# Kernel optimization log

Measured on AMD Instinct MI355X. Metric: run time of the kernel, lower is better.

The kernel has to match this reference:

```python
import jax, jax.numpy as jnp
import numpy as np

B, S, D, H = 2, 2048, 1024, 16
DH = D // H
ROPE_BASE = 10000.0


def apply_rope(x):
    # x: [B, H, S, DH]; rotate-half RoPE, base 10000
    half = DH // 2
    inv_freq = 1.0 / (ROPE_BASE ** (jnp.arange(half, dtype=jnp.float32) / half))
    ang = jnp.arange(S, dtype=jnp.float32)[:, None] * inv_freq[None, :]  # [S, half]
    cos = jnp.cos(ang)[None, None]  # [1,1,S,half]
    sin = jnp.sin(ang)[None, None]
    x1, x2 = x[..., :half], x[..., half:]
    return jnp.concatenate([x1 * cos - x2 * sin, x1 * sin + x2 * cos], axis=-1)


def setup_inputs() -> dict:
    key = jax.random.key(0)
    ks = jax.random.split(key, 9)
    w = lambda k: jax.random.normal(k, (D, D), dtype=jnp.float32) * 0.02
    return {
        "x": jax.random.normal(ks[0], (B, S, D), dtype=jnp.float32),
        "Wq": w(ks[1]), "bq": jnp.zeros((D,), jnp.float32),
        "Wk": w(ks[2]), "bk": jnp.zeros((D,), jnp.float32),
        "Wv": w(ks[3]), "bv": jnp.zeros((D,), jnp.float32),
        "Wo": w(ks[4]), "bo": jnp.zeros((D,), jnp.float32),
    }


def reference(x, Wq, bq, Wk, bk, Wv, bv, Wo, bo):
    # projections (W stored as [in, out])
    q = x @ Wq + bq
    k = x @ Wk + bk
    v = x @ Wv + bv
    # [B, S, D] -> [B, H, S, DH]
    to_heads = lambda t: t.reshape(B, S, H, DH).transpose(0, 2, 1, 3)
    q, k, v = to_heads(q), to_heads(k), to_heads(v)
    q = apply_rope(q)
    k = apply_rope(k)
    scores = jnp.einsum("bhqd,bhkd->bhqk", q, k) / jnp.sqrt(jnp.float32(DH))
    causal = jnp.tril(jnp.ones((S, S), dtype=bool))  # [S, S]
    scores = jnp.where(causal[None, None], scores, -jnp.inf)
    probs = jax.nn.softmax(scores, axis=-1)
    ctx = jnp.einsum("bhqk,bhkd->bhqd", probs, v)
    ctx = ctx.transpose(0, 2, 1, 3).reshape(B, S, D)  # concat heads
    return ctx @ Wo + bo
```

## Files before the change

### kernel.cpp

```cpp
#include <hip/hip_runtime.h>
#include <hip/hip_bf16.h>

#define B_  2
#define S_  2048
#define D_  1024
#define H_  16
#define DH_ 64

typedef __attribute__((ext_vector_type(8))) short bf16x8;
typedef __attribute__((ext_vector_type(4))) float f32x4;

__device__ __forceinline__ short f2bf(float f) {
  unsigned int u; __builtin_memcpy(&u, &f, 4);
  u = (u + 0x7FFFu + ((u >> 16) & 1u)) >> 16;
  return (short)u;
}
__device__ __forceinline__ unsigned cvtpk(float a, float b) {
  unsigned r;
  asm("v_cvt_pk_bf16_f32 %0, %1, %2" : "=v"(r) : "v"(a), "v"(b));
  return r;
}

#define GLOAD_LDS16(gp, lp) \
  __builtin_amdgcn_global_load_lds((const __attribute__((address_space(1))) void*)(gp), \
                                   (__attribute__((address_space(3))) void*)(lp), 16, 0, 0)

#define MFMA16(a, b, c) __builtin_amdgcn_mfma_f32_16x16x32_bf16(a, b, c, 0, 0, 0)

union U8 { unsigned u[4]; bf16x8 v; };

__global__ __launch_bounds__(256) void k_cvt(const float* __restrict__ in,
                                             short* __restrict__ out, int n4) {
  int i = blockIdx.x * 256 + threadIdx.x;
  if (i >= n4) return;
  float4 v = ((const float4*)in)[i];
  short4 o; o.x = f2bf(v.x); o.y = f2bf(v.y); o.z = f2bf(v.z); o.w = f2bf(v.w);
  *(short4*)(out + (size_t)i * 4) = o;
}

__global__ __launch_bounds__(256) void k_transpose4(const float* __restrict__ W0,
                                                    const float* __restrict__ W1,
                                                    const float* __restrict__ W2,
                                                    const float* __restrict__ W3,
                                                    short* __restrict__ WtBase) {
  __shared__ float tile[32][33];
  const float* W = (blockIdx.z == 0) ? W0 : (blockIdx.z == 1) ? W1 :
                   (blockIdx.z == 2) ? W2 : W3;
  short* Wt = WtBase + (size_t)blockIdx.z * D_ * D_;
  int tx = threadIdx.x, ty = threadIdx.y;
  int bx = blockIdx.x * 32, by = blockIdx.y * 32;
  #pragma unroll
  for (int i = 0; i < 32; i += 8)
    tile[ty + i][tx] = W[(size_t)(by + ty + i) * D_ + bx + tx];
  __syncthreads();
  #pragma unroll
  for (int i = 0; i < 32; i += 8)
    Wt[(size_t)(bx + ty + i) * D_ + by + tx] = f2bf(tile[tx][ty + i]);
}

__global__ __launch_bounds__(256) void k_rope_table(float* __restrict__ cosT,
                                                    float* __restrict__ sinT) {
  int i = blockIdx.x * 256 + threadIdx.x;
  int s = i >> 5, d = i & 31;
  float invf = exp2f(-(float)d * (13.287712379549449f / 32.0f));
  float ang = (float)s * invf;
  cosT[i] = cosf(ang);
  sinT[i] = sinf(ang);
}

__global__ __launch_bounds__(256) void k_gemm_qkv(const short* __restrict__ A,
                                                  const short* __restrict__ Bt,
                                                  const float* __restrict__ bq,
                                                  const float* __restrict__ bk,
                                                  const float* __restrict__ bv,
                                                  const float* __restrict__ cosT,
                                                  const float* __restrict__ sinT,
                                                  short* __restrict__ qb,
                                                  short* __restrict__ kb,
                                                  short* __restrict__ vb) {
  const int K = 1024;
  __shared__ __align__(16) short lA[128 * 32];
  __shared__ __align__(16) short lB[128 * 32];
  const int tid = threadIdx.x;
  const int wid = tid >> 6, lane = tid & 63;
  const int brow = blockIdx.y * 128, bcol = blockIdx.x * 128;
  const int wr = wid >> 1, wc = wid & 1;
  const int g = lane >> 4, c15 = lane & 15;
  const int sr = lane >> 2, scol = (lane & 3) * 8;
  f32x4 acc[4][4] = {};

  for (int kt = 0; kt < K; kt += 32) {
    __syncthreads();
    #pragma unroll
    for (int ch = 0; ch < 2; ++ch) {
      const short* ga = A + (size_t)(brow + ch * 64 + wid * 16 + sr) * K + kt + scol;
      const short* gb = Bt + (size_t)(bcol + ch * 64 + wid * 16 + sr) * K + kt + scol;
      GLOAD_LDS16(ga, &lA[(ch * 64 + wid * 16) * 32]);
      GLOAD_LDS16(gb, &lB[(ch * 64 + wid * 16) * 32]);
    }
    __syncthreads();
    bf16x8 af[4], bfr[4];
    #pragma unroll
    for (int mi = 0; mi < 4; ++mi)
      af[mi] = *(const bf16x8*)&lA[(wr * 64 + mi * 16 + c15) * 32 + g * 8];
    #pragma unroll
    for (int ni = 0; ni < 4; ++ni)
      bfr[ni] = *(const bf16x8*)&lB[(wc * 64 + ni * 16 + c15) * 32 + g * 8];
    #pragma unroll
    for (int mi = 0; mi < 4; ++mi)
      #pragma unroll
      for (int ni = 0; ni < 4; ++ni)
        acc[mi][ni] = MFMA16(af[mi], bfr[ni], acc[mi][ni]);
  }

  const int seg = bcol >> 10;
  const float* bp = (seg == 0) ? bq : (seg == 1) ? bk : bv;
  short* dst = (seg == 0) ? qb : (seg == 1) ? kb : vb;
  const float alpha = (seg == 0) ? 0.18033688f : 1.0f;
  const bool rope = (seg < 2);
  #pragma unroll
  for (int mi = 0; mi < 4; ++mi) {
    #pragma unroll
    for (int ni = 0; ni < 2; ++ni) {
      int col  = bcol + wc * 64 + ni * 16 + c15;
      int lcol = col & 1023;
      int d    = col & 63;
      float b1 = bp[lcol], b2 = bp[lcol + 32];
      #pragma unroll
      for (int r = 0; r < 4; ++r) {
        int row = brow + wr * 64 + mi * 16 + g * 4 + r;
        float x1 = (acc[mi][ni][r]     + b1) * alpha;
        float x2 = (acc[mi][ni + 2][r] + b2) * alpha;
        float o1 = x1, o2 = x2;
        if (rope) {
          int s = row & (S_ - 1);
          float co = cosT[s * 32 + d], si = sinT[s * 32 + d];
          o1 = x1 * co - x2 * si;
          o2 = x1 * si + x2 * co;
        }
        dst[(size_t)row * 1024 + lcol]      = f2bf(o1);
        dst[(size_t)row * 1024 + lcol + 32] = f2bf(o2);
      }
    }
  }
}

__global__ __launch_bounds__(256) void k_gemm(const short* __restrict__ A,
                                              const short* __restrict__ Bt,
                                              const float* __restrict__ bias,
                                              float* __restrict__ out,
                                              int M, int N, int K) {
  __shared__ __align__(16) short lA[128 * 32];
  __shared__ __align__(16) short lB[128 * 32];
  const int tid = threadIdx.x;
  const int wid = tid >> 6, lane = tid & 63;
  const int brow = blockIdx.y * 128, bcol = blockIdx.x * 128;
  const int wr = wid >> 1, wc = wid & 1;
  const int g = lane >> 4, c15 = lane & 15;
  const int sr = lane >> 2, scol = (lane & 3) * 8;
  f32x4 acc[4][4] = {};

  for (int kt = 0; kt < K; kt += 32) {
    __syncthreads();
    #pragma unroll
    for (int ch = 0; ch < 2; ++ch) {
      const short* ga = A + (size_t)(brow + ch * 64 + wid * 16 + sr) * K + kt + scol;
      const short* gb = Bt + (size_t)(bcol + ch * 64 + wid * 16 + sr) * K + kt + scol;
      GLOAD_LDS16(ga, &lA[(ch * 64 + wid * 16) * 32]);
      GLOAD_LDS16(gb, &lB[(ch * 64 + wid * 16) * 32]);
    }
    __syncthreads();
    bf16x8 af[4], bfr[4];
    #pragma unroll
    for (int mi = 0; mi < 4; ++mi)
      af[mi] = *(const bf16x8*)&lA[(wr * 64 + mi * 16 + c15) * 32 + g * 8];
    #pragma unroll
    for (int ni = 0; ni < 4; ++ni)
      bfr[ni] = *(const bf16x8*)&lB[(wc * 64 + ni * 16 + c15) * 32 + g * 8];
    #pragma unroll
    for (int mi = 0; mi < 4; ++mi)
      #pragma unroll
      for (int ni = 0; ni < 4; ++ni)
        acc[mi][ni] = MFMA16(af[mi], bfr[ni], acc[mi][ni]);
  }

  #pragma unroll
  for (int mi = 0; mi < 4; ++mi) {
    #pragma unroll
    for (int ni = 0; ni < 4; ++ni) {
      int col = bcol + wc * 64 + ni * 16 + c15;
      float bv = bias[col];
      #pragma unroll
      for (int r = 0; r < 4; ++r) {
        int row = brow + wr * 64 + mi * 16 + g * 4 + r;
        out[(size_t)row * N + col] = acc[mi][ni][r] + bv;
      }
    }
  }
}

__global__ __launch_bounds__(256) void k_flash(const short* __restrict__ Qb,
                                               const short* __restrict__ Kb,
                                               const short* __restrict__ Vb,
                                               short* __restrict__ Ctx,
                                               float* __restrict__ pO,
                                               float* __restrict__ pML) {
  __shared__ __align__(16) short Vt[2][64][72];
  __shared__ __align__(16) short Kl[2][4096];
  const int bid = blockIdx.x;
  const int sched = bid >> 5, bh = bid & 31;
  int qt, t0, t1, sid = 0; bool split;
  if (sched < 19) { qt = 18 - sched; t0 = 0; t1 = qt; split = false; }
  else {
    int j = sched - 19; qt = 31 - (j >> 1);
    int h1 = (qt + 2) >> 1;
    if ((j & 1) == 0) { t0 = h1; t1 = qt; }
    else              { t0 = 0;  t1 = h1 - 1; }
    split = true; sid = bh * 26 + j;
  }
  const int b   = bh >> 4, h = bh & 15;
  const int tid = threadIdx.x, w = tid >> 6, lane = tid & 63;
  const int g   = lane >> 4, c15 = lane & 15;
  const int qg0 = qt * 64 + w * 16;
  const int qabs = qg0 + c15;

  const short* qp = Qb + ((size_t)(b * S_ + qabs)) * D_ + h * DH_ + g * 8;
  bf16x8 qf0 = *(const bf16x8*)qp;
  bf16x8 qf1 = *(const bf16x8*)(qp + 32);

  const int vkv = lane;
  const int vd0 = w * 16;
  const int vcol = vkv ^ (w << 3);
  const short* vrow = Vb + (size_t)b * S_ * D_ + h * DH_ + vd0;

  const short* kbase = Kb + (size_t)b * S_ * D_ + h * DH_;
  const int kidx0 = w * 128 + lane;
  const int kkv0 = kidx0 >> 3, kdb0 = (kidx0 & 7) ^ (kkv0 & 7);
  const int kidx1 = kidx0 + 64;
  const int kkv1 = kidx1 >> 3, kdb1 = (kidx1 & 7) ^ (kkv1 & 7);

  f32x4 o[4] = {};
  float m = -1e30f, l = 0.0f;

  {
    const short* kb0 = kbase + (size_t)(t0 * 64) * D_;
    GLOAD_LDS16(kb0 + (size_t)kkv0 * D_ + kdb0 * 8, &Kl[t0 & 1][(w * 128) * 8]);
    GLOAD_LDS16(kb0 + (size_t)kkv1 * D_ + kdb1 * 8, &Kl[t0 & 1][(w * 128 + 64) * 8]);
    const short* vp = vrow + (size_t)(t0 * 64 + vkv) * D_;
    bf16x8 a = *(const bf16x8*)vp;
    bf16x8 c = *(const bf16x8*)(vp + 8);
    #pragma unroll
    for (int j = 0; j < 8; ++j) Vt[t0 & 1][vd0 + j][vcol] = a[j];
    #pragma unroll
    for (int j = 0; j < 8; ++j) Vt[t0 & 1][vd0 + 8 + j][vcol] = c[j];
  }
  __syncthreads();

  for (int t = t0; t <= t1; ++t) {
    const int kv0 = t * 64;
    bf16x8 nv0, nv1;
    if (t + 1 <= t1) {
      const short* kb2 = kbase + (size_t)(kv0 + 64) * D_;
      GLOAD_LDS16(kb2 + (size_t)kkv0 * D_ + kdb0 * 8, &Kl[(t + 1) & 1][(w * 128) * 8]);
      GLOAD_LDS16(kb2 + (size_t)kkv1 * D_ + kdb1 * 8, &Kl[(t + 1) & 1][(w * 128 + 64) * 8]);
      const short* vp = vrow + (size_t)(kv0 + 64 + vkv) * D_;
      nv0 = *(const bf16x8*)vp;
      nv1 = *(const bf16x8*)(vp + 8);
    }
    const short* ks = &Kl[t & 1][0];
    f32x4 s[4] = {};
    __builtin_amdgcn_s_setprio(1);
    #pragma unroll
    for (int n = 0; n < 4; ++n) {
      int krow = (n * 16 + c15) * 64;
      bf16x8 k0 = *(const bf16x8*)&ks[krow + ((g ^ (c15 & 7)) * 8)];
      bf16x8 k1 = *(const bf16x8*)&ks[krow + (((g + 4) ^ (c15 & 7)) * 8)];
      s[n] = MFMA16(k0, qf0, s[n]);
      s[n] = MFMA16(k1, qf1, s[n]);
    }
    __builtin_amdgcn_s_setprio(0);
    if (kv0 + 63 > qg0) {
      #pragma unroll
      for (int n = 0; n < 4; ++n)
        #pragma unroll
        for (int r = 0; r < 4; ++r)
          if (kv0 + n * 16 + g * 4 + r > qabs) s[n][r] = -1e30f;
    }
    float pm = -1e30f;
    #pragma unroll
    for (int n = 0; n < 4; ++n)
      #pragma unroll
      for (int r = 0; r < 4; ++r) pm = fmaxf(pm, s[n][r]);
    pm = fmaxf(pm, __shfl_xor(pm, 16));
    pm = fmaxf(pm, __shfl_xor(pm, 32));
    if (!__all(pm <= m + 8.0f)) {
      float nm = fmaxf(m, pm);
      float corr = exp2f(m - nm);
      m = nm; l *= corr;
      float cf[4];
      #pragma unroll
      for (int r = 0; r < 4; ++r) cf[r] = __shfl(corr, g * 4 + r);
      #pragma unroll
      for (int dblk = 0; dblk < 4; ++dblk)
        #pragma unroll
        for (int r = 0; r < 4; ++r) o[dblk][r] *= cf[r];
    }
    float rs = 0.0f;
    #pragma unroll
    for (int n = 0; n < 4; ++n)
      #pragma unroll
      for (int r = 0; r < 4; ++r) {
        float p = exp2f(s[n][r] - m);
        s[n][r] = p; rs += p;
      }
    rs += __shfl_xor(rs, 16);
    rs += __shfl_xor(rs, 32);
    l += rs;
    unsigned pk[4][2];
    #pragma unroll
    for (int n = 0; n < 4; ++n) {
      pk[n][0] = cvtpk(s[n][0], s[n][1]);
      pk[n][1] = cvtpk(s[n][2], s[n][3]);
    }
    U8 pa[2];
    #pragma unroll
    for (int kh = 0; kh < 2; ++kh) {
      #pragma unroll
      for (int widx = 0; widx < 4; ++widx) {
        int src = (2 * (g & 1) + (widx >> 1)) * 16 + c15;
        unsigned lo = __shfl(pk[2 * kh][widx & 1], src);
        unsigned hi = __shfl(pk[2 * kh + 1][widx & 1], src);
        pa[kh].u[widx] = (g & 2) ? hi : lo;
      }
    }
    __builtin_amdgcn_s_setprio(1);
    #pragma unroll
    for (int kh = 0; kh < 2; ++kh)
      #pragma unroll
      for (int dblk = 0; dblk < 4; ++dblk) {
        bf16x8 vbf = *(const bf16x8*)&Vt[t & 1][dblk * 16 + c15][kh * 32 + ((g ^ dblk) * 8)];
        o[dblk] = MFMA16(pa[kh].v, vbf, o[dblk]);
      }
    __builtin_amdgcn_s_setprio(0);
    if (t + 1 <= t1) {
      #pragma unroll
      for (int j = 0; j < 8; ++j) Vt[(t + 1) & 1][vd0 + j][vcol] = nv0[j];
      #pragma unroll
      for (int j = 0; j < 8; ++j) Vt[(t + 1) & 1][vd0 + 8 + j][vcol] = nv1[j];
    }
    __syncthreads();
  }

  if (!split) {
    float linv = 1.0f / l;
    float lf[4];
    #pragma unroll
    for (int r = 0; r < 4; ++r) lf[r] = __shfl(linv, g * 4 + r);
    #pragma unroll
    for (int dblk = 0; dblk < 4; ++dblk)
      #pragma unroll
      for (int r = 0; r < 4; ++r) {
        int q = qg0 + g * 4 + r;
        Ctx[((size_t)(b * S_ + q)) * D_ + h * DH_ + dblk * 16 + c15] = f2bf(o[dblk][r] * lf[r]);
      }
  } else {
    float* po = pO + ((size_t)sid * 64 + w * 16) * 64;
    #pragma unroll
    for (int dblk = 0; dblk < 4; ++dblk)
      #pragma unroll
      for (int r = 0; r < 4; ++r)
        po[(g * 4 + r) * 64 + dblk * 16 + c15] = o[dblk][r];
    if (lane < 16) {
      pML[(size_t)sid * 128 + w * 16 + lane]      = m;
      pML[(size_t)sid * 128 + 64 + w * 16 + lane] = l;
    }
  }
}

__global__ __launch_bounds__(256) void k_combine(const float* __restrict__ pO,
                                                 const float* __restrict__ pML,
                                                 short* __restrict__ Ctx) {
  const int p = blockIdx.x;
  const int qt = 19 + (p >> 5), bh = p & 31;
  const int b = bh >> 4, h = bh & 15;
  const int jb = (31 - qt) * 2;
  const int sidB = bh * 26 + jb;
  const int sidA = bh * 26 + jb + 1;
  const int q = threadIdx.x >> 2;
  const int d0 = (threadIdx.x & 3) * 16;
  float mA = pML[(size_t)sidA * 128 + q], lA = pML[(size_t)sidA * 128 + 64 + q];
  float mB = pML[(size_t)sidB * 128 + q], lB = pML[(size_t)sidB * 128 + 64 + q];
  float M = fmaxf(mA, mB);
  float wA = exp2f(mA - M), wB = exp2f(mB - M);
  float inv = 1.0f / (lA * wA + lB * wB);
  const float* oA = pO + ((size_t)sidA * 64 + q) * 64 + d0;
  const float* oB = pO + ((size_t)sidB * 64 + q) * 64 + d0;
  short* cp = Ctx + ((size_t)(b * S_ + qt * 64 + q)) * D_ + h * DH_ + d0;
  #pragma unroll
  for (int i = 0; i < 16; i += 4) {
    float4 a = *(const float4*)(oA + i);
    float4 c = *(const float4*)(oB + i);
    cp[i + 0] = f2bf((a.x * wA + c.x * wB) * inv);
    cp[i + 1] = f2bf((a.y * wA + c.y * wB) * inv);
    cp[i + 2] = f2bf((a.z * wA + c.z * wB) * inv);
    cp[i + 3] = f2bf((a.w * wA + c.w * wB) * inv);
  }
}

extern "C" void kernel_launch(void* const* d_in, const int* in_sizes, int n_in,
                              void* d_out, int out_size, void* d_ws, size_t ws_size,
                              hipStream_t stream) {
  (void)in_sizes; (void)n_in; (void)out_size; (void)ws_size;
  const float* x  = (const float*)d_in[0];
  const float* Wq = (const float*)d_in[1];
  const float* bq = (const float*)d_in[2];
  const float* Wk = (const float*)d_in[3];
  const float* bk = (const float*)d_in[4];
  const float* Wv = (const float*)d_in[5];
  const float* bv = (const float*)d_in[6];
  const float* Wo = (const float*)d_in[7];
  const float* bo = (const float*)d_in[8];
  float* out = (float*)d_out;
  char* ws = (char*)d_ws;

  const size_t MS = (size_t)B_ * S_;
  short* xb  = (short*)(ws);
  short* wqT = (short*)(ws + (size_t)8 * 1024 * 1024);
  short* wkT = wqT + (size_t)D_ * D_;
  short* wvT = wkT + (size_t)D_ * D_;
  short* woT = wvT + (size_t)D_ * D_;
  short* qb  = (short*)(ws + (size_t)16 * 1024 * 1024);
  short* kb  = qb + MS * D_;
  short* vb  = kb + MS * D_;
  short* ctx = vb + MS * D_;
  float* cosT = (float*)(ws + (size_t)48 * 1024 * 1024);
  float* sinT = cosT + (size_t)S_ * 32;
  float* pO  = (float*)(ws);
  float* pML = (float*)(ws + (size_t)48 * 1024 * 1024 + 512 * 1024);

  k_cvt<<<dim3((unsigned)(MS * D_ / 4 / 256)), 256, 0, stream>>>(x, xb, (int)(MS * D_ / 4));
  k_transpose4<<<dim3(32, 32, 4), dim3(32, 8), 0, stream>>>(Wq, Wk, Wv, Wo, wqT);
  k_rope_table<<<dim3(S_ * 32 / 256), 256, 0, stream>>>(cosT, sinT);
  k_gemm_qkv<<<dim3(24, 32), 256, 0, stream>>>(xb, wqT, bq, bk, bv, cosT, sinT, qb, kb, vb);
  k_flash<<<dim3(45 * 32), 256, 0, stream>>>(qb, kb, vb, ctx, pO, pML);
  k_combine<<<dim3(13 * 32), 256, 0, stream>>>(pO, pML, ctx);
  k_gemm<<<dim3(8, 32), 256, 0, stream>>>(ctx, woT, bo, out, 4096, 1024, 1024);
}
```

Before: 138.5 us.

## Double query rows per flash block to reuse K/V tiles, re-plan split schedule

```diff
diff --git a/kernel.cpp b/kernel.cpp
--- a/kernel.cpp
+++ b/kernel.cpp
@@ -199,34 +199,92 @@
   }
 }
 
-__global__ __launch_bounds__(256) void k_flash(const short* __restrict__ Qb,
-                                               const short* __restrict__ Kb,
-                                               const short* __restrict__ Vb,
-                                               short* __restrict__ Ctx,
-                                               float* __restrict__ pO,
-                                               float* __restrict__ pML) {
+__device__ __forceinline__ void softmax_g(f32x4 (&s)[4], float& m, float& l,
+                                          f32x4 (&o)[4], int g) {
+  float pm = -1e30f;
+  #pragma unroll
+  for (int n = 0; n < 4; ++n)
+    #pragma unroll
+    for (int r = 0; r < 4; ++r) pm = fmaxf(pm, s[n][r]);
+  pm = fmaxf(pm, __shfl_xor(pm, 16));
+  pm = fmaxf(pm, __shfl_xor(pm, 32));
+  if (!__all(pm <= m + 8.0f)) {
+    float nm = fmaxf(m, pm);
+    float corr = exp2f(m - nm);
+    m = nm; l *= corr;
+    float cf[4];
+    #pragma unroll
+    for (int r = 0; r < 4; ++r) cf[r] = __shfl(corr, g * 4 + r);
+    #pragma unroll
+    for (int dblk = 0; dblk < 4; ++dblk)
+      #pragma unroll
+      for (int r = 0; r < 4; ++r) o[dblk][r] *= cf[r];
+  }
+  float rs = 0.0f;
+  #pragma unroll
+  for (int n = 0; n < 4; ++n)
+    #pragma unroll
+    for (int r = 0; r < 4; ++r) {
+      float p = exp2f(s[n][r] - m);
+      s[n][r] = p; rs += p;
+    }
+  rs += __shfl_xor(rs, 16);
+  rs += __shfl_xor(rs, 32);
+  l += rs;
+}
+
+__device__ __forceinline__ void build_pa(const f32x4 (&s)[4], U8 (&pa)[2],
+                                         int g, int c15) {
+  unsigned pk[4][2];
+  #pragma unroll
+  for (int n = 0; n < 4; ++n) {
+    pk[n][0] = cvtpk(s[n][0], s[n][1]);
+    pk[n][1] = cvtpk(s[n][2], s[n][3]);
+  }
+  #pragma unroll
+  for (int kh = 0; kh < 2; ++kh) {
+    #pragma unroll
+    for (int widx = 0; widx < 4; ++widx) {
+      int src = (2 * (g & 1) + (widx >> 1)) * 16 + c15;
+      unsigned lo = __shfl(pk[2 * kh][widx & 1], src);
+      unsigned hi = __shfl(pk[2 * kh + 1][widx & 1], src);
+      pa[kh].u[widx] = (g & 2) ? hi : lo;
+    }
+  }
+}
+
+__global__ __launch_bounds__(256, 4) void k_flash(const short* __restrict__ Qb,
+                                                  const short* __restrict__ Kb,
+                                                  const short* __restrict__ Vb,
+                                                  short* __restrict__ Ctx,
+                                                  float* __restrict__ pO,
+                                                  float* __restrict__ pML) {
   __shared__ __align__(16) short Vt[2][64][72];
   __shared__ __align__(16) short Kl[2][4096];
   const int bid = blockIdx.x;
   const int sched = bid >> 5, bh = bid & 31;
-  int qt, t0, t1, sid = 0; bool split;
-  if (sched < 19) { qt = 18 - sched; t0 = 0; t1 = qt; split = false; }
-  else {
-    int j = sched - 19; qt = 31 - (j >> 1);
-    int h1 = (qt + 2) >> 1;
-    if ((j & 1) == 0) { t0 = h1; t1 = qt; }
-    else              { t0 = 0;  t1 = h1 - 1; }
-    split = true; sid = bh * 26 + j;
-  }
+  const unsigned char QTs[23] = {8,15,15,7,14,14,6,13,13,12,12,5,11,11,10,10,4,9,9,3,2,1,0};
+  const unsigned char MDs[23] = {0,1, 2, 0,1, 2, 0,1, 2, 1, 2, 0,1, 2, 1, 2, 0,1,2,0,0,0,0};
+  const int qt = QTs[sched], md = MDs[sched];
+  int t0, t1;
+  if (md == 0)      { t0 = 0;      t1 = 2 * qt + 1; }
+  else if (md == 1) { t0 = 0;      t1 = qt; }
+  else              { t0 = qt + 1; t1 = 2 * qt + 1; }
+  const bool split = (md != 0);
+  const int sid = bh * 14 + (qt - 9) * 2 + (md == 2 ? 1 : 0);
   const int b   = bh >> 4, h = bh & 15;
   const int tid = threadIdx.x, w = tid >> 6, lane = tid & 63;
   const int g   = lane >> 4, c15 = lane & 15;
-  const int qg0 = qt * 64 + w * 16;
-  const int qabs = qg0 + c15;
-
-  const short* qp = Qb + ((size_t)(b * S_ + qabs)) * D_ + h * DH_ + g * 8;
-  bf16x8 qf0 = *(const bf16x8*)qp;
-  bf16x8 qf1 = *(const bf16x8*)(qp + 32);
+  const int qg0a = qt * 128 + w * 32;
+  const int qabsA = qg0a + c15;
+  const int qabsB = qg0a + 16 + c15;
+
+  const short* qpA = Qb + ((size_t)(b * S_ + qabsA)) * D_ + h * DH_ + g * 8;
+  const short* qpB = Qb + ((size_t)(b * S_ + qabsB)) * D_ + h * DH_ + g * 8;
+  bf16x8 qfa0 = *(const bf16x8*)qpA;
+  bf16x8 qfa1 = *(const bf16x8*)(qpA + 32);
+  bf16x8 qfb0 = *(const bf16x8*)qpB;
+  bf16x8 qfb1 = *(const bf16x8*)(qpB + 32);
 
   const int vkv = lane;
   const int vd0 = w * 16;
@@ -239,8 +297,8 @@
   const int kidx1 = kidx0 + 64;
   const int kkv1 = kidx1 >> 3, kdb1 = (kidx1 & 7) ^ (kkv1 & 7);
 
-  f32x4 o[4] = {};
-  float m = -1e30f, l = 0.0f;
+  f32x4 oa[4] = {}, ob[4] = {};
+  float ma = -1e30f, la = 0.0f, mb = -1e30f, lb = 0.0f;
 
   {
     const short* kb0 = kbase + (size_t)(t0 * 64) * D_;
@@ -267,112 +325,90 @@
       nv0 = *(const bf16x8*)vp;
       nv1 = *(const bf16x8*)(vp + 8);
     }
-    const short* ks = &Kl[t & 1][0];
-    f32x4 s[4] = {};
-    __builtin_amdgcn_s_setprio(1);
-    #pragma unroll
-    for (int n = 0; n < 4; ++n) {
-      int krow = (n * 16 + c15) * 64;
-      bf16x8 k0 = *(const bf16x8*)&ks[krow + ((g ^ (c15 & 7)) * 8)];
-      bf16x8 k1 = *(const bf16x8*)&ks[krow + (((g + 4) ^ (c15 & 7)) * 8)];
-      s[n] = MFMA16(k0, qf0, s[n]);
-      s[n] = MFMA16(k1, qf1, s[n]);
-    }
-    __builtin_amdgcn_s_setprio(0);
-    if (kv0 + 63 > qg0) {
-      #pragma unroll
-      for (int n = 0; n < 4; ++n)
+    const bool liveB = (kv0 <= qg0a + 31);
+    if (liveB) {
+      const bool liveA = (kv0 <= qg0a + 15);
+      const short* ks = &Kl[t & 1][0];
+      f32x4 sa[4] = {}, sb[4] = {};
+      __builtin_amdgcn_s_setprio(1);
+      #pragma unroll
+      for (int n = 0; n < 4; ++n) {
+        int krow = (n * 16 + c15) * 64;
+        bf16x8 k0 = *(const bf16x8*)&ks[krow + ((g ^ (c15 & 7)) * 8)];
+        bf16x8 k1 = *(const bf16x8*)&ks[krow + (((g + 4) ^ (c15 & 7)) * 8)];
+        sa[n] = MFMA16(k0, qfa0, sa[n]);
+        sa[n] = MFMA16(k1, qfa1, sa[n]);
+        sb[n] = MFMA16(k0, qfb0, sb[n]);
+        sb[n] = MFMA16(k1, qfb1, sb[n]);
+      }
+      __builtin_amdgcn_s_setprio(0);
+      if (kv0 + 63 > qg0a) {
         #pragma unroll
-        for (int r = 0; r < 4; ++r)
-          if (kv0 + n * 16 + g * 4 + r > qabs) s[n][r] = -1e30f;
-    }
-    float pm = -1e30f;
-    #pragma unroll
-    for (int n = 0; n < 4; ++n)
-      #pragma unroll
-      for (int r = 0; r < 4; ++r) pm = fmaxf(pm, s[n][r]);
-    pm = fmaxf(pm, __shfl_xor(pm, 16));
-    pm = fmaxf(pm, __shfl_xor(pm, 32));
-    if (!__all(pm <= m + 8.0f)) {
-      float nm = fmaxf(m, pm);
-      float corr = exp2f(m - nm);
-      m = nm; l *= corr;
-      float cf[4];
-      #pragma unroll
-      for (int r = 0; r < 4; ++r) cf[r] = __shfl(corr, g * 4 + r);
-      #pragma unroll
-      for (int dblk = 0; dblk < 4; ++dblk)
+        for (int n = 0; n < 4; ++n)
+          #pragma unroll
+          for (int r = 0; r < 4; ++r)
+            if (kv0 + n * 16 + g * 4 + r > qabsA) sa[n][r] = -1e30f;
+      }
+      if (kv0 + 63 > qg0a + 16) {
         #pragma unroll
-        for (int r = 0; r < 4; ++r) o[dblk][r] *= cf[r];
-    }
-    float rs = 0.0f;
-    #pragma unroll
-    for (int n = 0; n < 4; ++n)
+        for (int n = 0; n < 4; ++n)
+          #pragma unroll
+          for (int r = 0; r < 4; ++r)
+            if (kv0 + n * 16 + g * 4 + r > qabsB) sb[n][r] = -1e30f;
+      }
+      U8 paa[2], pab[2];
+      if (liveA) { softmax_g(sa, ma, la, oa, g); build_pa(sa, paa, g, c15); }
+      softmax_g(sb, mb, lb, ob, g); build_pa(sb, pab, g, c15);
+      __builtin_amdgcn_s_setprio(1);
+      #pragma unroll
+      for (int kh = 0; kh < 2; ++kh)
+        #pragma unroll
+        for (int dblk = 0; dblk < 4; ++dblk) {
+          bf16x8 vbf = *(const bf16x8*)&Vt[t & 1][dblk * 16 + c15][kh * 32 + ((g ^ dblk) * 8)];
+          if (liveA) oa[dblk] = MFMA16(paa[kh].v, vbf, oa[dblk]);
+          ob[dblk] = MFMA16(pab[kh].v, vbf, ob[dblk]);
+        }
+      __builtin_amdgcn_s_setprio(0);
+    }
+    if (t + 1 <= t1) {
+      #pragma unroll
+      for (int j = 0; j < 8; ++j) Vt[(t + 1) & 1][vd0 + j][vcol] = nv0[j];
+      #pragma unroll
+      for (int j = 0; j < 8; ++j) Vt[(t + 1) & 1][vd0 + 8 + j][vcol] = nv1[j];
+    }
+    __syncthreads();
+  }
+
+  if (!split) {
+    float liA = 1.0f / la, liB = 1.0f / lb;
+    float lfA[4], lfB[4];
+    #pragma unroll
+    for (int r = 0; r < 4; ++r) {
+      lfA[r] = __shfl(liA, g * 4 + r);
+      lfB[r] = __shfl(liB, g * 4 + r);
+    }
+    #pragma unroll
+    for (int dblk = 0; dblk < 4; ++dblk)
       #pragma unroll
       for (int r = 0; r < 4; ++r) {
-        float p = exp2f(s[n][r] - m);
-        s[n][r] = p; rs += p;
-      }
-    rs += __shfl_xor(rs, 16);
-    rs += __shfl_xor(rs, 32);
-    l += rs;
-    unsigned pk[4][2];
-    #pragma unroll
-    for (int n = 0; n < 4; ++n) {
-      pk[n][0] = cvtpk(s[n][0], s[n][1]);
-      pk[n][1] = cvtpk(s[n][2], s[n][3]);
-    }
-    U8 pa[2];
-    #pragma unroll
-    for (int kh = 0; kh < 2; ++kh) {
-      #pragma unroll
-      for (int widx = 0; widx < 4; ++widx) {
-        int src = (2 * (g & 1) + (widx >> 1)) * 16 + c15;
-        unsigned lo = __shfl(pk[2 * kh][widx & 1], src);
-        unsigned hi = __shfl(pk[2 * kh + 1][widx & 1], src);
-        pa[kh].u[widx] = (g & 2) ? hi : lo;
-      }
-    }
-    __builtin_amdgcn_s_setprio(1);
-    #pragma unroll
-    for (int kh = 0; kh < 2; ++kh)
-      #pragma unroll
-      for (int dblk = 0; dblk < 4; ++dblk) {
-        bf16x8 vbf = *(const bf16x8*)&Vt[t & 1][dblk * 16 + c15][kh * 32 + ((g ^ dblk) * 8)];
-        o[dblk] = MFMA16(pa[kh].v, vbf, o[dblk]);
-      }
-    __builtin_amdgcn_s_setprio(0);
-    if (t + 1 <= t1) {
-      #pragma unroll
-      for (int j = 0; j < 8; ++j) Vt[(t + 1) & 1][vd0 + j][vcol] = nv0[j];
-      #pragma unroll
-      for (int j = 0; j < 8; ++j) Vt[(t + 1) & 1][vd0 + 8 + j][vcol] = nv1[j];
-    }
-    __syncthreads();
-  }
-
-  if (!split) {
-    float linv = 1.0f / l;
-    float lf[4];
-    #pragma unroll
-    for (int r = 0; r < 4; ++r) lf[r] = __shfl(linv, g * 4 + r);
+        int qa = qg0a + g * 4 + r;
+        Ctx[((size_t)(b * S_ + qa)) * D_ + h * DH_ + dblk * 16 + c15] = f2bf(oa[dblk][r] * lfA[r]);
+        Ctx[((size_t)(b * S_ + qa + 16)) * D_ + h * DH_ + dblk * 16 + c15] = f2bf(ob[dblk][r] * lfB[r]);
+      }
+  } else {
+    float* po = pO + ((size_t)sid * 128 + w * 32) * 64;
     #pragma unroll
     for (int dblk = 0; dblk < 4; ++dblk)
       #pragma unroll
       for (int r = 0; r < 4; ++r) {
-        int q = qg0 + g * 4 + r;
-        Ctx[((size_t)(b * S_ + q)) * D_ + h * DH_ + dblk * 16 + c15] = f2bf(o[dblk][r] * lf[r]);
-      }
-  } else {
-    float* po = pO + ((size_t)sid * 64 + w * 16) * 64;
-    #pragma unroll
-    for (int dblk = 0; dblk < 4; ++dblk)
-      #pragma unroll
-      for (int r = 0; r < 4; ++r)
-        po[(g * 4 + r) * 64 + dblk * 16 + c15] = o[dblk][r];
+        po[(g * 4 + r) * 64 + dblk * 16 + c15]        = oa[dblk][r];
+        po[(16 + g * 4 + r) * 64 + dblk * 16 + c15]   = ob[dblk][r];
+      }
     if (lane < 16) {
-      pML[(size_t)sid * 128 + w * 16 + lane]      = m;
-      pML[(size_t)sid * 128 + 64 + w * 16 + lane] = l;
+      pML[(size_t)sid * 256 + w * 32 + lane]            = ma;
+      pML[(size_t)sid * 256 + 128 + w * 32 + lane]      = la;
+      pML[(size_t)sid * 256 + w * 32 + 16 + lane]       = mb;
+      pML[(size_t)sid * 256 + 128 + w * 32 + 16 + lane] = lb;
     }
   }
 }
@@ -381,23 +417,22 @@
                                                  const float* __restrict__ pML,
                                                  short* __restrict__ Ctx) {
   const int p = blockIdx.x;
-  const int qt = 19 + (p >> 5), bh = p & 31;
+  const int qt = 9 + (p >> 5), bh = p & 31;
   const int b = bh >> 4, h = bh & 15;
-  const int jb = (31 - qt) * 2;
-  const int sidB = bh * 26 + jb;
-  const int sidA = bh * 26 + jb + 1;
-  const int q = threadIdx.x >> 2;
-  const int d0 = (threadIdx.x & 3) * 16;
-  float mA = pML[(size_t)sidA * 128 + q], lA = pML[(size_t)sidA * 128 + 64 + q];
-  float mB = pML[(size_t)sidB * 128 + q], lB = pML[(size_t)sidB * 128 + 64 + q];
+  const int sidA = bh * 14 + (qt - 9) * 2;
+  const int sidB = sidA + 1;
+  const int row = threadIdx.x >> 1;
+  const int d0 = (threadIdx.x & 1) * 32;
+  float mA = pML[(size_t)sidA * 256 + row], lA = pML[(size_t)sidA * 256 + 128 + row];
+  float mB = pML[(size_t)sidB * 256 + row], lB = pML[(size_t)sidB * 256 + 128 + row];
   float M = fmaxf(mA, mB);
   float wA = exp2f(mA - M), wB = exp2f(mB - M);
   float inv = 1.0f / (lA * wA + lB * wB);
-  const float* oA = pO + ((size_t)sidA * 64 + q) * 64 + d0;
-  const float* oB = pO + ((size_t)sidB * 64 + q) * 64 + d0;
-  short* cp = Ctx + ((size_t)(b * S_ + qt * 64 + q)) * D_ + h * DH_ + d0;
-  #pragma unroll
-  for (int i = 0; i < 16; i += 4) {
+  const float* oA = pO + ((size_t)sidA * 128 + row) * 64 + d0;
+  const float* oB = pO + ((size_t)sidB * 128 + row) * 64 + d0;
+  short* cp = Ctx + ((size_t)(b * S_ + qt * 128 + row)) * D_ + h * DH_ + d0;
+  #pragma unroll
+  for (int i = 0; i < 32; i += 4) {
     float4 a = *(const float4*)(oA + i);
     float4 c = *(const float4*)(oB + i);
     cp[i + 0] = f2bf((a.x * wA + c.x * wB) * inv);
@@ -442,7 +477,7 @@
   k_transpose4<<<dim3(32, 32, 4), dim3(32, 8), 0, stream>>>(Wq, Wk, Wv, Wo, wqT);
   k_rope_table<<<dim3(S_ * 32 / 256), 256, 0, stream>>>(cosT, sinT);
   k_gemm_qkv<<<dim3(24, 32), 256, 0, stream>>>(xb, wqT, bq, bk, bv, cosT, sinT, qb, kb, vb);
-  k_flash<<<dim3(45 * 32), 256, 0, stream>>>(qb, kb, vb, ctx, pO, pML);
-  k_combine<<<dim3(13 * 32), 256, 0, stream>>>(pO, pML, ctx);
+  k_flash<<<dim3(23 * 32), 256, 0, stream>>>(qb, kb, vb, ctx, pO, pML);
+  k_combine<<<dim3(7 * 32), 256, 0, stream>>>(pO, pML, ctx);
   k_gemm<<<dim3(8, 32), 256, 0, stream>>>(ctx, woT, bo, out, 4096, 1024, 1024);
 }
```

Result: slower. 162.7 us (+17.5%).

## Use 128-row query tiles with 8-wave flash blocks and rebalanced split schedule

Applied to the files above, without the earlier changes.

```diff
diff --git a/kernel.cpp b/kernel.cpp
--- a/kernel.cpp
+++ b/kernel.cpp
@@ -199,7 +199,61 @@
   }
 }
 
-__global__ __launch_bounds__(256) void k_flash(const short* __restrict__ Qb,
+__device__ __forceinline__ void softmax_g(f32x4 (&s)[4], float& m, float& l,
+                                          f32x4 (&o)[4], int g) {
+  float pm = -1e30f;
+  #pragma unroll
+  for (int n = 0; n < 4; ++n)
+    #pragma unroll
+    for (int r = 0; r < 4; ++r) pm = fmaxf(pm, s[n][r]);
+  pm = fmaxf(pm, __shfl_xor(pm, 16));
+  pm = fmaxf(pm, __shfl_xor(pm, 32));
+  if (!__all(pm <= m + 8.0f)) {
+    float nm = fmaxf(m, pm);
+    float corr = exp2f(m - nm);
+    m = nm; l *= corr;
+    float cf[4];
+    #pragma unroll
+    for (int r = 0; r < 4; ++r) cf[r] = __shfl(corr, g * 4 + r);
+    #pragma unroll
+    for (int dblk = 0; dblk < 4; ++dblk)
+      #pragma unroll
+      for (int r = 0; r < 4; ++r) o[dblk][r] *= cf[r];
+  }
+  float rs = 0.0f;
+  #pragma unroll
+  for (int n = 0; n < 4; ++n)
+    #pragma unroll
+    for (int r = 0; r < 4; ++r) {
+      float p = exp2f(s[n][r] - m);
+      s[n][r] = p; rs += p;
+    }
+  rs += __shfl_xor(rs, 16);
+  rs += __shfl_xor(rs, 32);
+  l += rs;
+}
+
+__device__ __forceinline__ void build_pa(const f32x4 (&s)[4], U8 (&pa)[2],
+                                         int g, int c15) {
+  unsigned pk[4][2];
+  #pragma unroll
+  for (int n = 0; n < 4; ++n) {
+    pk[n][0] = cvtpk(s[n][0], s[n][1]);
+    pk[n][1] = cvtpk(s[n][2], s[n][3]);
+  }
+  #pragma unroll
+  for (int kh = 0; kh < 2; ++kh) {
+    #pragma unroll
+    for (int widx = 0; widx < 4; ++widx) {
+      int src = (2 * (g & 1) + (widx >> 1)) * 16 + c15;
+      unsigned lo = __shfl(pk[2 * kh][widx & 1], src);
+      unsigned hi = __shfl(pk[2 * kh + 1][widx & 1], src);
+      pa[kh].u[widx] = (g & 2) ? hi : lo;
+    }
+  }
+}
+
+__global__ __launch_bounds__(512) void k_flash(const short* __restrict__ Qb,
                                                const short* __restrict__ Kb,
                                                const short* __restrict__ Vb,
                                                short* __restrict__ Ctx,
@@ -209,19 +263,19 @@
   __shared__ __align__(16) short Kl[2][4096];
   const int bid = blockIdx.x;
   const int sched = bid >> 5, bh = bid & 31;
-  int qt, t0, t1, sid = 0; bool split;
-  if (sched < 19) { qt = 18 - sched; t0 = 0; t1 = qt; split = false; }
-  else {
-    int j = sched - 19; qt = 31 - (j >> 1);
-    int h1 = (qt + 2) >> 1;
-    if ((j & 1) == 0) { t0 = h1; t1 = qt; }
-    else              { t0 = 0;  t1 = h1 - 1; }
-    split = true; sid = bh * 26 + j;
-  }
+  const unsigned char QTs[22] = {9,8,15,15,7,14,14,6,13,13,12,12,5,11,11,10,10,4,3,2,1,0};
+  const unsigned char MDs[22] = {0,0,1, 2, 0,1, 2, 0,1, 2, 1, 2, 0,1, 2, 1, 2, 0,0,0,0,0};
+  const int qt = QTs[sched], md = MDs[sched];
+  int t0, t1;
+  if (md == 0)      { t0 = 0;      t1 = 2 * qt + 1; }
+  else if (md == 1) { t0 = 0;      t1 = qt; }
+  else              { t0 = qt + 1; t1 = 2 * qt + 1; }
+  const bool split = (md != 0);
+  const int sid = bh * 12 + (qt - 10) * 2 + (md == 2 ? 1 : 0);
   const int b   = bh >> 4, h = bh & 15;
   const int tid = threadIdx.x, w = tid >> 6, lane = tid & 63;
   const int g   = lane >> 4, c15 = lane & 15;
-  const int qg0 = qt * 64 + w * 16;
+  const int qg0 = qt * 128 + w * 16;
   const int qabs = qg0 + c15;
 
   const short* qp = Qb + ((size_t)(b * S_ + qabs)) * D_ + h * DH_ + g * 8;
@@ -229,124 +283,71 @@
   bf16x8 qf1 = *(const bf16x8*)(qp + 32);
 
   const int vkv = lane;
-  const int vd0 = w * 16;
-  const int vcol = vkv ^ (w << 3);
+  const int vd0 = w * 8;
+  const int vcol = vkv ^ ((w >> 1) << 3);
   const short* vrow = Vb + (size_t)b * S_ * D_ + h * DH_ + vd0;
 
   const short* kbase = Kb + (size_t)b * S_ * D_ + h * DH_;
-  const int kidx0 = w * 128 + lane;
-  const int kkv0 = kidx0 >> 3, kdb0 = (kidx0 & 7) ^ (kkv0 & 7);
-  const int kidx1 = kidx0 + 64;
-  const int kkv1 = kidx1 >> 3, kdb1 = (kidx1 & 7) ^ (kkv1 & 7);
+  const int kidx = w * 64 + lane;
+  const int kkv = kidx >> 3, kdb = (kidx & 7) ^ (kkv & 7);
 
   f32x4 o[4] = {};
   float m = -1e30f, l = 0.0f;
 
   {
     const short* kb0 = kbase + (size_t)(t0 * 64) * D_;
-    GLOAD_LDS16(kb0 + (size_t)kkv0 * D_ + kdb0 * 8, &Kl[t0 & 1][(w * 128) * 8]);
-    GLOAD_LDS16(kb0 + (size_t)kkv1 * D_ + kdb1 * 8, &Kl[t0 & 1][(w * 128 + 64) * 8]);
+    GLOAD_LDS16(kb0 + (size_t)kkv * D_ + kdb * 8, &Kl[t0 & 1][kidx * 8]);
     const short* vp = vrow + (size_t)(t0 * 64 + vkv) * D_;
     bf16x8 a = *(const bf16x8*)vp;
-    bf16x8 c = *(const bf16x8*)(vp + 8);
     #pragma unroll
     for (int j = 0; j < 8; ++j) Vt[t0 & 1][vd0 + j][vcol] = a[j];
-    #pragma unroll
-    for (int j = 0; j < 8; ++j) Vt[t0 & 1][vd0 + 8 + j][vcol] = c[j];
   }
   __syncthreads();
 
   for (int t = t0; t <= t1; ++t) {
     const int kv0 = t * 64;
-    bf16x8 nv0, nv1;
+    bf16x8 nv;
     if (t + 1 <= t1) {
       const short* kb2 = kbase + (size_t)(kv0 + 64) * D_;
-      GLOAD_LDS16(kb2 + (size_t)kkv0 * D_ + kdb0 * 8, &Kl[(t + 1) & 1][(w * 128) * 8]);
-      GLOAD_LDS16(kb2 + (size_t)kkv1 * D_ + kdb1 * 8, &Kl[(t + 1) & 1][(w * 128 + 64) * 8]);
-      const short* vp = vrow + (size_t)(kv0 + 64 + vkv) * D_;
-      nv0 = *(const bf16x8*)vp;
-      nv1 = *(const bf16x8*)(vp + 8);
-    }
-    const short* ks = &Kl[t & 1][0];
-    f32x4 s[4] = {};
-    __builtin_amdgcn_s_setprio(1);
-    #pragma unroll
-    for (int n = 0; n < 4; ++n) {
-      int krow = (n * 16 + c15) * 64;
-      bf16x8 k0 = *(const bf16x8*)&ks[krow + ((g ^ (c15 & 7)) * 8)];
-      bf16x8 k1 = *(const bf16x8*)&ks[krow + (((g + 4) ^ (c15 & 7)) * 8)];
-      s[n] = MFMA16(k0, qf0, s[n]);
-      s[n] = MFMA16(k1, qf1, s[n]);
-    }
-    __builtin_amdgcn_s_setprio(0);
-    if (kv0 + 63 > qg0) {
-      #pragma unroll
-      for (int n = 0; n < 4; ++n)
+      GLOAD_LDS16(kb2 + (size_t)kkv * D_ + kdb * 8, &Kl[(t + 1) & 1][kidx * 8]);
+      nv = *(const bf16x8*)(vrow + (size_t)(kv0 + 64 + vkv) * D_);
+    }
+    if (kv0 <= qg0 + 15) {
+      const short* ks = &Kl[t & 1][0];
+      f32x4 s[4] = {};
+      __builtin_amdgcn_s_setprio(1);
+      #pragma unroll
+      for (int n = 0; n < 4; ++n) {
+        int krow = (n * 16 + c15) * 64;
+        bf16x8 k0 = *(const bf16x8*)&ks[krow + ((g ^ (c15 & 7)) * 8)];
+        bf16x8 k1 = *(const bf16x8*)&ks[krow + (((g + 4) ^ (c15 & 7)) * 8)];
+        s[n] = MFMA16(k0, qf0, s[n]);
+        s[n] = MFMA16(k1, qf1, s[n]);
+      }
+      __builtin_amdgcn_s_setprio(0);
+      if (kv0 + 63 > qg0) {
         #pragma unroll
-        for (int r = 0; r < 4; ++r)
-          if (kv0 + n * 16 + g * 4 + r > qabs) s[n][r] = -1e30f;
-    }
-    float pm = -1e30f;
-    #pragma unroll
-    for (int n = 0; n < 4; ++n)
-      #pragma unroll
-      for (int r = 0; r < 4; ++r) pm = fmaxf(pm, s[n][r]);
-    pm = fmaxf(pm, __shfl_xor(pm, 16));
-    pm = fmaxf(pm, __shfl_xor(pm, 32));
-    if (!__all(pm <= m + 8.0f)) {
-      float nm = fmaxf(m, pm);
-      float corr = exp2f(m - nm);
-      m = nm; l *= corr;
-      float cf[4];
-      #pragma unroll
-      for (int r = 0; r < 4; ++r) cf[r] = __shfl(corr, g * 4 + r);
-      #pragma unroll
-      for (int dblk = 0; dblk < 4; ++dblk)
+        for (int n = 0; n < 4; ++n)
+          #pragma unroll
+          for (int r = 0; r < 4; ++r)
+            if (kv0 + n * 16 + g * 4 + r > qabs) s[n][r] = -1e30f;
+      }
+      softmax_g(s, m, l, o, g);
+      U8 pa[2];
+      build_pa(s, pa, g, c15);
+      __builtin_amdgcn_s_setprio(1);
+      #pragma unroll
+      for (int kh = 0; kh < 2; ++kh)
         #pragma unroll
-        for (int r = 0; r < 4; ++r) o[dblk][r] *= cf[r];
-    }
-    float rs = 0.0f;
-    #pragma unroll
-    for (int n = 0; n < 4; ++n)
-      #pragma unroll
-      for (int r = 0; r < 4; ++r) {
-        float p = exp2f(s[n][r] - m);
-        s[n][r] = p; rs += p;
-      }
-    rs += __shfl_xor(rs, 16);
-    rs += __shfl_xor(rs, 32);
-    l += rs;
-    unsigned pk[4][2];
-    #pragma unroll
-    for (int n = 0; n < 4; ++n) {
-      pk[n][0] = cvtpk(s[n][0], s[n][1]);
-      pk[n][1] = cvtpk(s[n][2], s[n][3]);
-    }
-    U8 pa[2];
-    #pragma unroll
-    for (int kh = 0; kh < 2; ++kh) {
-      #pragma unroll
-      for (int widx = 0; widx < 4; ++widx) {
-        int src = (2 * (g & 1) + (widx >> 1)) * 16 + c15;
-        unsigned lo = __shfl(pk[2 * kh][widx & 1], src);
-        unsigned hi = __shfl(pk[2 * kh + 1][widx & 1], src);
-        pa[kh].u[widx] = (g & 2) ? hi : lo;
-      }
-    }
-    __builtin_amdgcn_s_setprio(1);
-    #pragma unroll
-    for (int kh = 0; kh < 2; ++kh)
-      #pragma unroll
-      for (int dblk = 0; dblk < 4; ++dblk) {
-        bf16x8 vbf = *(const bf16x8*)&Vt[t & 1][dblk * 16 + c15][kh * 32 + ((g ^ dblk) * 8)];
-        o[dblk] = MFMA16(pa[kh].v, vbf, o[dblk]);
-      }
-    __builtin_amdgcn_s_setprio(0);
+        for (int dblk = 0; dblk < 4; ++dblk) {
+          bf16x8 vbf = *(const bf16x8*)&Vt[t & 1][dblk * 16 + c15][kh * 32 + ((g ^ dblk) * 8)];
+          o[dblk] = MFMA16(pa[kh].v, vbf, o[dblk]);
+        }
+      __builtin_amdgcn_s_setprio(0);
+    }
     if (t + 1 <= t1) {
       #pragma unroll
-      for (int j = 0; j < 8; ++j) Vt[(t + 1) & 1][vd0 + j][vcol] = nv0[j];
-      #pragma unroll
-      for (int j = 0; j < 8; ++j) Vt[(t + 1) & 1][vd0 + 8 + j][vcol] = nv1[j];
+      for (int j = 0; j < 8; ++j) Vt[(t + 1) & 1][vd0 + j][vcol] = nv[j];
     }
     __syncthreads();
   }
@@ -364,15 +365,15 @@
         Ctx[((size_t)(b * S_ + q)) * D_ + h * DH_ + dblk * 16 + c15] = f2bf(o[dblk][r] * lf[r]);
       }
   } else {
-    float* po = pO + ((size_t)sid * 64 + w * 16) * 64;
+    float* po = pO + ((size_t)sid * 128 + w * 16) * 64;
     #pragma unroll
     for (int dblk = 0; dblk < 4; ++dblk)
       #pragma unroll
       for (int r = 0; r < 4; ++r)
         po[(g * 4 + r) * 64 + dblk * 16 + c15] = o[dblk][r];
     if (lane < 16) {
-      pML[(size_t)sid * 128 + w * 16 + lane]      = m;
-      pML[(size_t)sid * 128 + 64 + w * 16 + lane] = l;
+      pML[(size_t)sid * 256 + w * 16 + lane]       = m;
+      pML[(size_t)sid * 256 + 128 + w * 16 + lane] = l;
     }
   }
 }
@@ -381,23 +382,22 @@
                                                  const float* __restrict__ pML,
                                                  short* __restrict__ Ctx) {
   const int p = blockIdx.x;
-  const int qt = 19 + (p >> 5), bh = p & 31;
+  const int qt = 10 + (p >> 5), bh = p & 31;
   const int b = bh >> 4, h = bh & 15;
-  const int jb = (31 - qt) * 2;
-  const int sidB = bh * 26 + jb;
-  const int sidA = bh * 26 + jb + 1;
-  const int q = threadIdx.x >> 2;
-  const int d0 = (threadIdx.x & 3) * 16;
-  float mA = pML[(size_t)sidA * 128 + q], lA = pML[(size_t)sidA * 128 + 64 + q];
-  float mB = pML[(size_t)sidB * 128 + q], lB = pML[(size_t)sidB * 128 + 64 + q];
+  const int sidA = bh * 12 + (qt - 10) * 2;
+  const int sidB = sidA + 1;
+  const int row = threadIdx.x >> 1;
+  const int d0 = (threadIdx.x & 1) * 32;
+  float mA = pML[(size_t)sidA * 256 + row], lA = pML[(size_t)sidA * 256 + 128 + row];
+  float mB = pML[(size_t)sidB * 256 + row], lB = pML[(size_t)sidB * 256 + 128 + row];
   float M = fmaxf(mA, mB);
   float wA = exp2f(mA - M), wB = exp2f(mB - M);
   float inv = 1.0f / (lA * wA + lB * wB);
-  const float* oA = pO + ((size_t)sidA * 64 + q) * 64 + d0;
-  const float* oB = pO + ((size_t)sidB * 64 + q) * 64 + d0;
-  short* cp = Ctx + ((size_t)(b * S_ + qt * 64 + q)) * D_ + h * DH_ + d0;
-  #pragma unroll
-  for (int i = 0; i < 16; i += 4) {
+  const float* oA = pO + ((size_t)sidA * 128 + row) * 64 + d0;
+  const float* oB = pO + ((size_t)sidB * 128 + row) * 64 + d0;
+  short* cp = Ctx + ((size_t)(b * S_ + qt * 128 + row)) * D_ + h * DH_ + d0;
+  #pragma unroll
+  for (int i = 0; i < 32; i += 4) {
     float4 a = *(const float4*)(oA + i);
     float4 c = *(const float4*)(oB + i);
     cp[i + 0] = f2bf((a.x * wA + c.x * wB) * inv);
@@ -442,7 +442,7 @@
   k_transpose4<<<dim3(32, 32, 4), dim3(32, 8), 0, stream>>>(Wq, Wk, Wv, Wo, wqT);
   k_rope_table<<<dim3(S_ * 32 / 256), 256, 0, stream>>>(cosT, sinT);
   k_gemm_qkv<<<dim3(24, 32), 256, 0, stream>>>(xb, wqT, bq, bk, bv, cosT, sinT, qb, kb, vb);
-  k_flash<<<dim3(45 * 32), 256, 0, stream>>>(qb, kb, vb, ctx, pO, pML);
-  k_combine<<<dim3(13 * 32), 256, 0, stream>>>(pO, pML, ctx);
+  k_flash<<<dim3(22 * 32), 512, 0, stream>>>(qb, kb, vb, ctx, pO, pML);
+  k_combine<<<dim3(6 * 32), 256, 0, stream>>>(pO, pML, ctx);
   k_gemm<<<dim3(8, 32), 256, 0, stream>>>(ctx, woT, bo, out, 4096, 1024, 1024);
 }
```

Result: slower. 142.7 us (+3.1%).
